# Optimization experiments

Measured on AMD Instinct MI355X. Metric: run time of the kernel, lower is better.

The kernel has to match this reference:

```python
import jax, jax.numpy as jnp
import numpy as np

N, IN_F, OUT_F, K = 256, 8192, 8320, 16
J = OUT_F - IN_F  # 128


def setup_inputs() -> dict:
    key = jax.random.key(0)
    k1, k2 = jax.random.split(key)
    tensor = jax.random.normal(k1, (N, IN_F), dtype=jnp.float32)
    T = jax.random.normal(k2, (IN_F, J, K), dtype=jnp.float32)
    return {"tensor": tensor, "T": T}


def reference(tensor, T):
    # flatten(start_dim=1) is identity for rank-2 input
    x = tensor.reshape(tensor.shape[0], -1)            # [N, IN_F]
    feats = jnp.einsum('ni,ijk->njk', x, T)            # [N, J, K]
    # pairwise L1 across batch: [N,1,J,K] - [N,J,K] -> [N,N,J,K]
    diff = jnp.abs(feats[:, None, :, :] - feats[None, :, :, :])
    l1 = jnp.sum(diff, axis=3)                         # [N, N, J]
    diversity = jnp.sum(jnp.exp(-l1), axis=1)          # [N, J]
    return jnp.concatenate((x, diversity), axis=1)     # [N, IN_F + J]
```

## Files before the change

kernel.cpp:

```cpp
#include <hip/hip_runtime.h>

typedef unsigned int  u32;
typedef unsigned short u16;

typedef __bf16 bf16x8 __attribute__((ext_vector_type(8)));
typedef float  floatx4 __attribute__((ext_vector_type(4)));

#define N_ROWS 256
#define IN_F   8192
#define OUT_F  8320
#define JDIM   128
#define KDIM   16
#define JK     2048

#define BM     256
#define BN     64
#define BK     64
#define XSTRIDE 72
#define WSTRIDE 72

#define SLAB_U16   (N_ROWS * JK)
#define JSLICE_U16 (N_ROWS * KDIM)

__device__ __forceinline__ u16 f2bf(float f) {
    u32 u = __float_as_uint(f);
    return (u16)((u + 0x7fffu + ((u >> 16) & 1u)) >> 16);
}
__device__ __forceinline__ float bf2f(u16 h) { return __uint_as_float(((u32)h) << 16); }

__device__ __forceinline__ u32 cvtpk(float lo, float hi) {
    u32 d;
    asm("v_cvt_pk_bf16_f32 %0, %1, %2" : "=v"(d) : "v"(lo), "v"(hi));
    return d;
}

template<int S>
__global__ __launch_bounds__(256, 2) void gemm_kernel(const float* __restrict__ X,
                                                      const float* __restrict__ W,
                                                      u16* __restrict__ slabs,
                                                      float* __restrict__ out)
{
    constexpr int KCH   = IN_F / S;
    constexpr int ITERS = KCH >> 6;

    __shared__ __align__(16) u16 xs[BM * XSTRIDE];
    __shared__ __align__(16) u16 wt[BN * WSTRIDE];

    const int tid  = threadIdx.x;
    const int lane = tid & 63;
    const int wave = tid >> 6;
    const int c0   = blockIdx.x * BN;
    const int s    = blockIdx.y;
    const int k0base = s * KCH;

    if (s == 0) {
        int g = blockIdx.x * 256 + tid;
        int r2 = g >> 5, j4 = g & 31;
        reinterpret_cast<float4*>(out + (size_t)r2 * OUT_F + IN_F)[j4] =
            make_float4(0.f, 0.f, 0.f, 0.f);
    }

    floatx4 acc[4][4] = {};

    const int xr = lane >> 3;
    const int xc = lane & 7;
    const float* xptr = X + (size_t)(wave * 64 + xr) * IN_F + k0base + xc * 8;

    const int wk = (tid >> 4) << 2;
    const int wc = (tid & 15) << 2;
    const float* wptr = W + (size_t)(k0base + wk) * JK + c0 + wc;

    float4 xreg[16];
    float4 wreg[4];
    #pragma unroll
    for (int i = 0; i < 8; ++i) {
        const float* p = xptr + (size_t)i * 8 * IN_F;
        xreg[2 * i]     = ((const float4*)p)[0];
        xreg[2 * i + 1] = ((const float4*)p)[1];
    }
    #pragma unroll
    for (int r = 0; r < 4; ++r)
        wreg[r] = *(const float4*)(wptr + (size_t)r * JK);

    for (int it = 0; it < ITERS; ++it) {
        __syncthreads();

        #pragma unroll
        for (int i = 0; i < 8; ++i) {
            int row = wave * 64 + i * 8 + xr;
            uint4 q;
            q.x = cvtpk(xreg[2 * i].x,     xreg[2 * i].y);
            q.y = cvtpk(xreg[2 * i].z,     xreg[2 * i].w);
            q.z = cvtpk(xreg[2 * i + 1].x, xreg[2 * i + 1].y);
            q.w = cvtpk(xreg[2 * i + 1].z, xreg[2 * i + 1].w);
            *(uint4*)&xs[row * XSTRIDE + xc * 8] = q;
        }

        {
            const float* wr = (const float*)wreg;
            #pragma unroll
            for (int i = 0; i < 4; ++i) {
                uint2 v;
                v.x = cvtpk(wr[0 * 4 + i], wr[1 * 4 + i]);
                v.y = cvtpk(wr[2 * 4 + i], wr[3 * 4 + i]);
                *(uint2*)&wt[(wc + i) * WSTRIDE + wk] = v;
            }
        }
        __syncthreads();

        if (it + 1 < ITERS) {
            const float* xn = xptr + (size_t)(it + 1) * BK;
            #pragma unroll
            for (int i = 0; i < 8; ++i) {
                const float* p = xn + (size_t)i * 8 * IN_F;
                xreg[2 * i]     = ((const float4*)p)[0];
                xreg[2 * i + 1] = ((const float4*)p)[1];
            }
            const float* wn = wptr + (size_t)(it + 1) * BK * JK;
            #pragma unroll
            for (int r = 0; r < 4; ++r)
                wreg[r] = *(const float4*)(wn + (size_t)r * JK);
        }

        const int mrow = lane & 15;
        const int q    = lane >> 4;
        #pragma unroll
        for (int h = 0; h < 2; ++h) {
            bf16x8 a[4], b[4];
            #pragma unroll
            for (int rt = 0; rt < 4; ++rt) {
                int rl = wave * 64 + rt * 16 + mrow;
                a[rt] = *reinterpret_cast<const bf16x8*>(&xs[rl * XSTRIDE + (h * 4 + q) * 8]);
            }
            #pragma unroll
            for (int ct = 0; ct < 4; ++ct) {
                int col = ct * 16 + mrow;
                b[ct] = *reinterpret_cast<const bf16x8*>(&wt[col * WSTRIDE + (h * 4 + q) * 8]);
            }
            #pragma unroll
            for (int rt = 0; rt < 4; ++rt)
                #pragma unroll
                for (int ct = 0; ct < 4; ++ct)
                    acc[rt][ct] = __builtin_amdgcn_mfma_f32_16x16x32_bf16(a[rt], b[ct], acc[rt][ct], 0, 0, 0);
        }
    }

    const int qe = lane >> 4;
    const int cl = lane & 15;
    u16* sp = slabs + (size_t)s * SLAB_U16;
    #pragma unroll
    for (int rt = 0; rt < 4; ++rt)
        #pragma unroll
        for (int ct = 0; ct < 4; ++ct) {
            int j = (c0 >> 4) + ct;
            #pragma unroll
            for (int r = 0; r < 4; ++r) {
                int row = wave * 64 + rt * 16 + qe * 4 + r;
                sp[(size_t)j * JSLICE_U16 + row * KDIM + cl] = f2bf(acc[rt][ct][r]);
            }
        }
}

template<int S>
__global__ __launch_bounds__(256) void fused_rp_kernel(const u16* __restrict__ slabs,
                                                       const float* __restrict__ X,
                                                       float* __restrict__ out)
{
    const int j  = blockIdx.x;
    const int mq = blockIdx.y;
    const int n  = threadIdx.x;
    const int lin = blockIdx.y * JDIM + blockIdx.x;
    const int g0  = lin * 256 + n;

    __shared__ float F[N_ROWS * KDIM];

    const u16* base = slabs + (size_t)j * JSLICE_U16 + n * KDIM;

    float f[16];
    #pragma unroll
    for (int k = 0; k < 16; ++k) f[k] = 0.f;

    #pragma unroll
    for (int so = 0; so < S; so += 4) {
        uint4 va[4], vb[4];
        #pragma unroll
        for (int i = 0; i < 4 && so + i < S; ++i) {
            const u16* p = base + (size_t)(so + i) * SLAB_U16;
            va[i] = *(const uint4*)p;
            vb[i] = *(const uint4*)(p + 8);
        }
        #pragma unroll
        for (int i = 0; i < 4 && so + i < S; ++i) {
            const u16* ha = (const u16*)&va[i];
            const u16* hb = (const u16*)&vb[i];
            #pragma unroll
            for (int e = 0; e < 8; ++e) {
                f[e]     += bf2f(ha[e]);
                f[8 + e] += bf2f(hb[e]);
            }
        }
    }

    float4* Fp = (float4*)&F[n * KDIM];
    Fp[0] = make_float4(f[0],  f[1],  f[2],  f[3]);
    Fp[1] = make_float4(f[4],  f[5],  f[6],  f[7]);
    Fp[2] = make_float4(f[8],  f[9],  f[10], f[11]);
    Fp[3] = make_float4(f[12], f[13], f[14], f[15]);

    float4 cp[4];
    #pragma unroll
    for (int i = 0; i < 4; ++i)
        cp[i] = reinterpret_cast<const float4*>(X)[g0 + i * 131072];

    __syncthreads();

    float accum = 0.f;
    const int m0 = mq * 64;
    #pragma unroll 2
    for (int m = 0; m < 64; ++m) {
        const float* Fm = &F[(m0 + m) * KDIM];
        float l1 = 0.f;
        #pragma unroll
        for (int k = 0; k < 16; ++k) l1 += fabsf(f[k] - Fm[k]);
        accum += exp2f(-1.4426950408889634f * l1);
    }
    atomicAdd(&out[(size_t)n * OUT_F + IN_F + j], accum);

    #pragma unroll
    for (int i = 0; i < 4; ++i) {
        int t = g0 + i * 131072;
        int row = t >> 11, c4 = t & 2047;
        reinterpret_cast<float4*>(out + (size_t)row * OUT_F)[c4] = cp[i];
    }
}

extern "C" void kernel_launch(void* const* d_in, const int* in_sizes, int n_in,
                              void* d_out, int out_size, void* d_ws, size_t ws_size,
                              hipStream_t stream)
{
    const float* X = (const float*)d_in[0];
    const float* T = (const float*)d_in[1];
    float* out = (float*)d_out;

    u16* slabs = (u16*)d_ws;

    int S = 16;
    if (ws_size < (size_t)16 * SLAB_U16 * 2) S = 8;
    if (ws_size < (size_t)8  * SLAB_U16 * 2) S = 4;

    if (S == 16) {
        gemm_kernel<16><<<dim3(JK / BN, 16), 256, 0, stream>>>(X, T, slabs, out);
        fused_rp_kernel<16><<<dim3(JDIM, 4), 256, 0, stream>>>(slabs, X, out);
    } else if (S == 8) {
        gemm_kernel<8><<<dim3(JK / BN, 8), 256, 0, stream>>>(X, T, slabs, out);
        fused_rp_kernel<8><<<dim3(JDIM, 4), 256, 0, stream>>>(slabs, X, out);
    } else {
        gemm_kernel<4><<<dim3(JK / BN, 4), 256, 0, stream>>>(X, T, slabs, out);
        fused_rp_kernel<4><<<dim3(JDIM, 4), 256, 0, stream>>>(slabs, X, out);
    }
}
```

Before: 154.6 us.

## Stream X tiles directly to LDS as fp32 with XOR swizzle, remap GEMM blocks

The X tile is now loaded straight from global memory into shared memory as fp32 using global_load_lds, with an XOR swizzle to avoid bank conflicts. The bf16 conversion moves to the point where each MFMA fragment is read. This removes the register staging of X and the earlier register-level prefetch. The GEMM grid becomes 1D, with a block-index remap that groups K-split slices, presumably for cache or XCD locality. In exchange the X load is no longer overlapped with the previous iteration's MFMAs, and shared memory per block grows to about 73KB, which still allows two blocks per CU.

```diff
diff --git a/kernel.cpp b/kernel.cpp
--- a/kernel.cpp
+++ b/kernel.cpp
@@ -16,11 +16,13 @@
 #define BM     256
 #define BN     64
 #define BK     64
-#define XSTRIDE 72
 #define WSTRIDE 72
 
 #define SLAB_U16   (N_ROWS * JK)
 #define JSLICE_U16 (N_ROWS * KDIM)
+
+typedef const __attribute__((address_space(1))) u32 gu32;
+typedef __attribute__((address_space(3))) u32 su32;
 
 __device__ __forceinline__ u16 f2bf(float f) {
     u32 u = __float_as_uint(f);
@@ -43,18 +45,31 @@
     constexpr int KCH   = IN_F / S;
     constexpr int ITERS = KCH >> 6;
 
-    __shared__ __align__(16) u16 xs[BM * XSTRIDE];
-    __shared__ __align__(16) u16 wt[BN * WSTRIDE];
+    __shared__ __align__(16) float xsf[BM * BK];
+    __shared__ __align__(16) u16   wt[BN * WSTRIDE];
 
     const int tid  = threadIdx.x;
     const int lane = tid & 63;
     const int wave = tid >> 6;
-    const int c0   = blockIdx.x * BN;
-    const int s    = blockIdx.y;
+
+    int xblk, s;
+    {
+        int lin = blockIdx.x;
+        if constexpr (S == 16) {
+            int rem = lin >> 3;
+            xblk = rem & 31;
+            s = ((lin & 7) << 1) | (rem >> 5);
+        } else if constexpr (S == 8) {
+            s = lin & 7; xblk = lin >> 3;
+        } else {
+            xblk = lin & 31; s = lin >> 5;
+        }
+    }
+    const int c0     = xblk * BN;
     const int k0base = s * KCH;
 
     if (s == 0) {
-        int g = blockIdx.x * 256 + tid;
+        int g = xblk * 256 + tid;
         int r2 = g >> 5, j4 = g & 31;
         reinterpret_cast<float4*>(out + (size_t)r2 * OUT_F + IN_F)[j4] =
             make_float4(0.f, 0.f, 0.f, 0.f);
@@ -62,38 +77,29 @@
 
     floatx4 acc[4][4] = {};
 
-    const int xr = lane >> 3;
-    const int xc = lane & 7;
-    const float* xptr = X + (size_t)(wave * 64 + xr) * IN_F + k0base + xc * 8;
+    const int row_in = lane >> 4;
+    const int slot   = lane & 15;
 
     const int wk = (tid >> 4) << 2;
     const int wc = (tid & 15) << 2;
     const float* wptr = W + (size_t)(k0base + wk) * JK + c0 + wc;
 
-    float4 xreg[16];
     float4 wreg[4];
-    #pragma unroll
-    for (int i = 0; i < 8; ++i) {
-        const float* p = xptr + (size_t)i * 8 * IN_F;
-        xreg[2 * i]     = ((const float4*)p)[0];
-        xreg[2 * i + 1] = ((const float4*)p)[1];
-    }
     #pragma unroll
     for (int r = 0; r < 4; ++r)
         wreg[r] = *(const float4*)(wptr + (size_t)r * JK);
 
     for (int it = 0; it < ITERS; ++it) {
+        const int k0 = k0base + it * BK;
         __syncthreads();
 
         #pragma unroll
-        for (int i = 0; i < 8; ++i) {
-            int row = wave * 64 + i * 8 + xr;
-            uint4 q;
-            q.x = cvtpk(xreg[2 * i].x,     xreg[2 * i].y);
-            q.y = cvtpk(xreg[2 * i].z,     xreg[2 * i].w);
-            q.z = cvtpk(xreg[2 * i + 1].x, xreg[2 * i + 1].y);
-            q.w = cvtpk(xreg[2 * i + 1].z, xreg[2 * i + 1].w);
-            *(uint4*)&xs[row * XSTRIDE + xc * 8] = q;
+        for (int g = 0; g < 16; ++g) {
+            int rbase = wave * 64 + g * 4;
+            int gch   = slot ^ (4 * (g & 3) + row_in);
+            const float* gp = X + (size_t)(rbase + row_in) * IN_F + k0 + gch * 4;
+            u32* lp = (u32*)&xsf[rbase * BK];
+            __builtin_amdgcn_global_load_lds((gu32*)gp, (su32*)lp, 16, 0, 0);
         }
 
         {
@@ -109,13 +115,6 @@
         __syncthreads();
 
         if (it + 1 < ITERS) {
-            const float* xn = xptr + (size_t)(it + 1) * BK;
-            #pragma unroll
-            for (int i = 0; i < 8; ++i) {
-                const float* p = xn + (size_t)i * 8 * IN_F;
-                xreg[2 * i]     = ((const float4*)p)[0];
-                xreg[2 * i + 1] = ((const float4*)p)[1];
-            }
             const float* wn = wptr + (size_t)(it + 1) * BK * JK;
             #pragma unroll
             for (int r = 0; r < 4; ++r)
@@ -130,7 +129,17 @@
             #pragma unroll
             for (int rt = 0; rt < 4; ++rt) {
                 int rl = wave * 64 + rt * 16 + mrow;
-                a[rt] = *reinterpret_cast<const bf16x8*>(&xs[rl * XSTRIDE + (h * 4 + q) * 8]);
+                int t2 = (h * 4 + q) * 2;
+                int s0 = t2 ^ mrow;
+                int s1 = s0 ^ 1;
+                float4 u0 = *(const float4*)&xsf[rl * BK + s0 * 4];
+                float4 u1 = *(const float4*)&xsf[rl * BK + s1 * 4];
+                union { u32 u[4]; bf16x8 v; } pk;
+                pk.u[0] = cvtpk(u0.x, u0.y);
+                pk.u[1] = cvtpk(u0.z, u0.w);
+                pk.u[2] = cvtpk(u1.x, u1.y);
+                pk.u[3] = cvtpk(u1.z, u1.w);
+                a[rt] = pk.v;
             }
             #pragma unroll
             for (int ct = 0; ct < 4; ++ct) {
@@ -249,13 +258,13 @@
     if (ws_size < (size_t)8  * SLAB_U16 * 2) S = 4;
 
     if (S == 16) {
-        gemm_kernel<16><<<dim3(JK / BN, 16), 256, 0, stream>>>(X, T, slabs, out);
+        gemm_kernel<16><<<512, 256, 0, stream>>>(X, T, slabs, out);
         fused_rp_kernel<16><<<dim3(JDIM, 4), 256, 0, stream>>>(slabs, X, out);
     } else if (S == 8) {
-        gemm_kernel<8><<<dim3(JK / BN, 8), 256, 0, stream>>>(X, T, slabs, out);
+        gemm_kernel<8><<<256, 256, 0, stream>>>(X, T, slabs, out);
         fused_rp_kernel<8><<<dim3(JDIM, 4), 256, 0, stream>>>(slabs, X, out);
     } else {
-        gemm_kernel<4><<<dim3(JK / BN, 4), 256, 0, stream>>>(X, T, slabs, out);
+        gemm_kernel<4><<<128, 256, 0, stream>>>(X, T, slabs, out);
         fused_rp_kernel<4><<<dim3(JDIM, 4), 256, 0, stream>>>(slabs, X, out);
     }
 }
```

Measured after the change: 142.3 us. 7.9% less time.
